# Kernel optimization log

Measured on AMD Instinct MI355X. Metric: run time of the kernel, lower is better.

## Reference

```python
import jax, jax.numpy as jnp
import numpy as np
import math

B, S, D, H, L, V = 16, 512, 1024, 16, 128, 32000
DH = D // H


def _posenc(s, d):
    pos = np.arange(s, dtype=np.float32)[:, None]
    div = np.exp(np.arange(0, d, 2, dtype=np.float32) * (-math.log(10000.0) / d))
    pe = np.zeros((s, d), dtype=np.float32)
    pe[:, 0::2] = np.sin(pos * div)
    pe[:, 1::2] = np.cos(pos * div)
    return jnp.asarray(pe)


def _ln(x, g, b):
    m = jnp.mean(x, axis=-1, keepdims=True)
    v = jnp.mean((x - m) ** 2, axis=-1, keepdims=True)
    return (x - m) / jnp.sqrt(v + 1e-5) * g + b


def setup_inputs():
    key = jax.random.key(0)
    ks = jax.random.split(key, 16)
    w = lambda k, *sh: 0.02 * jax.random.normal(k, sh, dtype=jnp.float32)
    return {
        'x': jax.random.randint(ks[0], (B, S), 0, V),
        'embed': w(ks[1], V, D),
        'Wq': w(ks[2], D, D), 'bq': jnp.zeros((D,), jnp.float32),
        'Wk': w(ks[3], D, D), 'bk': jnp.zeros((D,), jnp.float32),
        'Wv': w(ks[4], D, D), 'bv': jnp.zeros((D,), jnp.float32),
        'Wo': w(ks[5], D, D), 'bo': jnp.zeros((D,), jnp.float32),
        'g1': jnp.ones((D,), jnp.float32), 'be1': jnp.zeros((D,), jnp.float32),
        'W1': w(ks[6], D, D), 'bf1': jnp.zeros((D,), jnp.float32),
        'W2': w(ks[7], D, D), 'bf2': jnp.zeros((D,), jnp.float32),
        'g2': jnp.ones((D,), jnp.float32), 'be2': jnp.zeros((D,), jnp.float32),
        'g3': jnp.ones((D,), jnp.float32), 'be3': jnp.zeros((D,), jnp.float32),
        'Wmu': w(ks[8], D, L), 'bmu': jnp.zeros((L,), jnp.float32),
        'Wsig': w(ks[9], D, L), 'bsig': jnp.zeros((L,), jnp.float32),
        'eps': jax.random.normal(ks[10], (B, S, L), dtype=jnp.float32),
    }


def reference(x, embed, Wq, bq, Wk, bk, Wv, bv, Wo, bo, g1, be1, W1, bf1, W2, bf2,
              g2, be2, g3, be3, Wmu, bmu, Wsig, bsig, eps):
    h = embed[x] * jnp.asarray(D ** 0.5, jnp.float32)          # [B,S,D]
    h = h + _posenc(S, D)                                       # dropout = identity (eval)
    h = _ln(h, g1, be1)
    # attention (faithful to source: raw reshape head-split, scale = dh/2)
    Q = (h @ Wq + bq).reshape(B, H, S, DH)
    K = (h @ Wk + bk).reshape(B, H, S, DH)
    Vv = (h @ Wv + bv).reshape(B, H, S, DH)
    scores = jnp.einsum('bhqd,bhkd->bhqk', Q, K) / (DH / 2.0)
    attn = jax.nn.softmax(scores, axis=-1)
    ctx = jnp.einsum('bhqk,bhkd->bhqd', attn, Vv).reshape(B, S, D)
    ctx = ctx @ Wo + bo
    h = h + ctx
    h = _ln(h, g2, be2)
    f = jax.nn.leaky_relu(h @ W1 + bf1, 0.01) @ W2 + bf2
    h = f + f                                                    # source: x = ffn(x); x = x + drop2(x)
    h = _ln(h, g3, be3)
    mu = h @ Wmu + bmu
    sigma = jnp.exp(h @ Wsig + bsig)
    z = mu + sigma * eps
    return z
```

## Files before the change

### kernel.cpp

```cpp
#include <hip/hip_runtime.h>
#include <cstdint>


typedef __bf16 bf16;
typedef __bf16 bf16x8 __attribute__((ext_vector_type(8)));
typedef __bf16 bf16x4 __attribute__((ext_vector_type(4)));
typedef float f32x4 __attribute__((ext_vector_type(4)));

#define MFMA16(a, b, c) __builtin_amdgcn_mfma_f32_16x16x32_bf16((a), (b), (c), 0, 0, 0)

#if __has_builtin(__builtin_amdgcn_exp2f)
#define EXP2F(x) __builtin_amdgcn_exp2f(x)
#else
#define EXP2F(x) exp2f(x)
#endif

__device__ __forceinline__ void async16(const bf16* g, bf16* l) {
  __builtin_amdgcn_global_load_lds(
      (const __attribute__((address_space(1))) unsigned int*)g,
      (__attribute__((address_space(3))) unsigned int*)l, 16, 0, 0);
}

struct TP6 {
  const float* src[6];
  bf16* dst[6];
};
__global__ __launch_bounds__(256) void transpose6_kernel(TP6 p) {
  const float* __restrict__ W = p.src[blockIdx.z];
  bf16* __restrict__ Wt = p.dst[blockIdx.z];
  __shared__ float tile[64][65];
  const int tk = blockIdx.x * 64, tn = blockIdx.y * 64;
  const int a = threadIdx.x >> 6, b = threadIdx.x & 63;
#pragma unroll
  for (int i = 0; i < 16; ++i) {
    int k = a + i * 4;
    tile[k][b] = W[(size_t)(tk + k) * 1024 + tn + b];
  }
  __syncthreads();
#pragma unroll
  for (int i = 0; i < 16; ++i) {
    int n = a + i * 4;
    Wt[(size_t)(tn + n) * 1024 + tk + b] = (bf16)tile[b][n];
  }
}

__global__ __launch_bounds__(256) void transpose_kernel(const float* __restrict__ W,
                                                        bf16* __restrict__ Wt,
                                                        int K, int N) {
  __shared__ float tile[64][65];
  const int tk = blockIdx.x * 64, tn = blockIdx.y * 64;
  const int a = threadIdx.x >> 6, b = threadIdx.x & 63;
#pragma unroll
  for (int i = 0; i < 16; ++i) {
    int k = a + i * 4;
    tile[k][b] = W[(size_t)(tk + k) * N + tn + b];
  }
  __syncthreads();
#pragma unroll
  for (int i = 0; i < 16; ++i) {
    int n = a + i * 4;
    Wt[(size_t)(tn + n) * K + tk + b] = (bf16)tile[b][n];
  }
}

__global__ __launch_bounds__(256) void embed_ln_kernel(const int* __restrict__ x,
                                                       const float* __restrict__ emb,
                                                       const float* __restrict__ g,
                                                       const float* __restrict__ be,
                                                       bf16* __restrict__ obf,
                                                       float* __restrict__ of) {
  const int row = blockIdx.x;
  const int s = row & 511;
  const int t = x[row];
  const int tid = threadIdx.x;
  const int c = tid * 4;
  const float4 e = *(const float4*)(emb + (size_t)t * 1024 + c);
  const float ev[4] = {e.x, e.y, e.z, e.w};
  float o[4];
#pragma unroll
  for (int j = 0; j < 4; ++j) {
    int cc = c + j;
    float freq = __expf((float)(cc & ~1) * (-9.210340371976184f / 1024.0f));
    float ang = (float)s * freq;
    float pe = (cc & 1) ? cosf(ang) : sinf(ang);
    o[j] = ev[j] * 32.0f + pe;
  }
  float sm = o[0] + o[1] + o[2] + o[3];
  float q = o[0] * o[0] + o[1] * o[1] + o[2] * o[2] + o[3] * o[3];
#pragma unroll
  for (int off = 32; off > 0; off >>= 1) {
    sm += __shfl_down(sm, off);
    q += __shfl_down(q, off);
  }
  __shared__ float rs[4], rq[4];
  const int w = tid >> 6, lane = tid & 63;
  if (lane == 0) { rs[w] = sm; rq[w] = q; }
  __syncthreads();
  const float S = rs[0] + rs[1] + rs[2] + rs[3];
  const float Qs = rq[0] + rq[1] + rq[2] + rq[3];
  const float mean = S * (1.0f / 1024.0f);
  const float var = Qs * (1.0f / 1024.0f) - mean * mean;
  const float rstd = rsqrtf(var + 1e-5f);
  const float4 gv = ((const float4*)g)[tid];
  const float4 bv = ((const float4*)be)[tid];
  const float gvv[4] = {gv.x, gv.y, gv.z, gv.w};
  const float bvv[4] = {bv.x, bv.y, bv.z, bv.w};
  float y[4];
#pragma unroll
  for (int j = 0; j < 4; ++j) y[j] = (o[j] - mean) * rstd * gvv[j] + bvv[j];
  bf16x4 ob = {(bf16)y[0], (bf16)y[1], (bf16)y[2], (bf16)y[3]};
  ((bf16x4*)(obf + (size_t)row * 1024))[tid] = ob;
  float4 o4;  o4.x = y[0]; o4.y = y[1]; o4.z = y[2]; o4.w = y[3];
  ((float4*)(of + (size_t)row * 1024))[tid] = o4;
}

__global__ __launch_bounds__(256) void ln_kernel(const float* __restrict__ in,
                                                 const float* __restrict__ g,
                                                 const float* __restrict__ be,
                                                 bf16* __restrict__ obf,
                                                 float* __restrict__ of) {
  const int row = blockIdx.x;
  const int tid = threadIdx.x;
  const float4 v = ((const float4*)(in + (size_t)row * 1024))[tid];
  float s = v.x + v.y + v.z + v.w;
  float q = v.x * v.x + v.y * v.y + v.z * v.z + v.w * v.w;
#pragma unroll
  for (int off = 32; off > 0; off >>= 1) {
    s += __shfl_down(s, off);
    q += __shfl_down(q, off);
  }
  __shared__ float rs[4], rq[4];
  const int w = tid >> 6, lane = tid & 63;
  if (lane == 0) { rs[w] = s; rq[w] = q; }
  __syncthreads();
  const float S = rs[0] + rs[1] + rs[2] + rs[3];
  const float Qs = rq[0] + rq[1] + rq[2] + rq[3];
  const float mean = S * (1.0f / 1024.0f);
  const float var = Qs * (1.0f / 1024.0f) - mean * mean;
  const float rstd = rsqrtf(var + 1e-5f);
  const float4 gv = ((const float4*)g)[tid];
  const float4 bv = ((const float4*)be)[tid];
  const float y0 = (v.x - mean) * rstd * gv.x + bv.x;
  const float y1 = (v.y - mean) * rstd * gv.y + bv.y;
  const float y2 = (v.z - mean) * rstd * gv.z + bv.z;
  const float y3 = (v.w - mean) * rstd * gv.w + bv.w;
  bf16x4 ob = {(bf16)y0, (bf16)y1, (bf16)y2, (bf16)y3};
  ((bf16x4*)(obf + (size_t)row * 1024))[tid] = ob;
  if (of) {
    float4 o4;  o4.x = y0; o4.y = y1; o4.z = y2; o4.w = y3;
    ((float4*)(of + (size_t)row * 1024))[tid] = o4;
  }
}

template <int MODE>
__global__ __launch_bounds__(256) void gemm_kernel(const bf16* __restrict__ A,
                                                   const bf16* __restrict__ Bt,
                                                   const float* __restrict__ bias,
                                                   void* __restrict__ outv,
                                                   const float* __restrict__ resid,
                                                   int M, int N, int K) {
  __shared__ __attribute__((aligned(16))) bf16 Asm[128 * 32];
  __shared__ __attribute__((aligned(16))) bf16 Bsm[128 * 32];
  const int tid = threadIdx.x;
  const int wv = tid >> 6, lane = tid & 63;
  const int quad = lane >> 4, l15 = lane & 15;
  const int m0 = blockIdx.x * 128, n0 = blockIdx.y * 128;
  const int wm = wv & 1, wn = wv >> 1;

  f32x4 acc[4][4];
#pragma unroll
  for (int i = 0; i < 4; ++i)
#pragma unroll
    for (int j = 0; j < 4; ++j) acc[i][j] = {0.f, 0.f, 0.f, 0.f};

  const int r0 = tid >> 2, c0 = ((tid & 3) ^ ((r0 >> 1) & 3)) * 8;
  const int r1 = (tid + 256) >> 2, c1 = ((tid & 3) ^ ((r1 >> 1) & 3)) * 8;
  const bf16* Ag0 = A + (size_t)(m0 + r0) * K + c0;
  const bf16* Ag1 = A + (size_t)(m0 + r1) * K + c1;
  const bf16* Bg0 = Bt + (size_t)(n0 + r0) * K + c0;
  const bf16* Bg1 = Bt + (size_t)(n0 + r1) * K + c1;
  bf16* lA0 = &Asm[tid * 8];
  bf16* lA1 = &Asm[(tid + 256) * 8];
  bf16* lB0 = &Bsm[tid * 8];
  bf16* lB1 = &Bsm[(tid + 256) * 8];

  for (int k0 = 0; k0 < K; k0 += 32) {
    async16(Ag0 + k0, lA0);
    async16(Ag1 + k0, lA1);
    async16(Bg0 + k0, lB0);
    async16(Bg1 + k0, lB1);
    __syncthreads();
    bf16x8 af[4], bfr[4];
#pragma unroll
    for (int mi = 0; mi < 4; ++mi) {
      const int row = wm * 64 + mi * 16 + l15;
      af[mi] = *(const bf16x8*)(&Asm[(row * 4 + (quad ^ ((row >> 1) & 3))) * 8]);
    }
#pragma unroll
    for (int ni = 0; ni < 4; ++ni) {
      const int row = wn * 64 + ni * 16 + l15;
      bfr[ni] = *(const bf16x8*)(&Bsm[(row * 4 + (quad ^ ((row >> 1) & 3))) * 8]);
    }
#pragma unroll
    for (int mi = 0; mi < 4; ++mi)
#pragma unroll
      for (int ni = 0; ni < 4; ++ni)
        acc[mi][ni] = MFMA16(af[mi], bfr[ni], acc[mi][ni]);
    __syncthreads();
  }

  float* outf = (float*)outv;
  bf16* outb = (bf16*)outv;
#pragma unroll
  for (int ni = 0; ni < 4; ++ni) {
    const int col = n0 + wn * 64 + ni * 16 + l15;
    float bv;
    if constexpr (MODE == 5)
      bv = (col < 128) ? bias[col] : resid[col - 128];
    else
      bv = bias[col];
#pragma unroll
    for (int mi = 0; mi < 4; ++mi) {
#pragma unroll
      for (int r = 0; r < 4; ++r) {
        const int row = m0 + wm * 64 + mi * 16 + quad * 4 + r;
        const size_t idx = (size_t)row * N + col;
        float v = acc[mi][ni][r] + bv;
        if constexpr (MODE == 0) outb[idx] = (bf16)v;
        else if constexpr (MODE == 1) outf[idx] = v + resid[idx];
        else if constexpr (MODE == 2) outb[idx] = (bf16)(v > 0.f ? v : 0.01f * v);
        else if constexpr (MODE == 3) outf[idx] = 2.0f * v;
        else outf[idx] = v;
      }
    }
  }
}

__global__ __launch_bounds__(256) void vtrans_kernel(const bf16* __restrict__ Vb,
                                                     bf16* __restrict__ VtG) {
  __shared__ float t[64][65];
  const int bh = blockIdx.x, kt = blockIdx.y;
  const int tid = threadIdx.x;
  const bf16* src = Vb + (size_t)bh * 32768 + (size_t)kt * 4096;
#pragma unroll
  for (int i = 0; i < 2; ++i) {
    int s = i * 256 + tid;
    int r = s >> 3, c = (s & 7) * 8;
    bf16x8 v = *(const bf16x8*)(src + (size_t)s * 8);
#pragma unroll
    for (int j = 0; j < 8; ++j) t[r][c + j] = (float)v[j];
  }
  __syncthreads();
  bf16* dst = VtG + (size_t)bh * 32768 + kt * 64;
#pragma unroll
  for (int i = 0; i < 2; ++i) {
    int s = i * 256 + tid;
    int d = s >> 3, kc = (s & 7) * 8;
    bf16 tmp[8];
#pragma unroll
    for (int j = 0; j < 8; ++j) tmp[j] = (bf16)t[kc + j][d];
    *(uint4*)(dst + (size_t)d * 512 + kc) = *(const uint4*)tmp;
  }
}

__global__ __launch_bounds__(256) void attn_kernel(const bf16* __restrict__ Qg,
                                                   const bf16* __restrict__ Kg,
                                                   const bf16* __restrict__ Vt,
                                                   bf16* __restrict__ ctx) {
  __shared__ __attribute__((aligned(16))) bf16 Ksm[128 * 64];
  __shared__ __attribute__((aligned(16))) bf16 Vsm[64 * 128];
  __shared__ __attribute__((aligned(16))) bf16 Psm[4][16 * 128];
  const int tid = threadIdx.x;
  const int w = tid >> 6, lane = tid & 63;
  const int quad = lane >> 4, l15 = lane & 15;
  const int bh = blockIdx.x;
  const size_t base = (size_t)bh * 32768;
  const bf16* Vth = Vt + base;
  const int qbase = blockIdx.y * 128 + w * 32;
  const f32x4 fz = {0.f, 0.f, 0.f, 0.f};

  bf16x8 a[2][2];
#pragma unroll
  for (int qt = 0; qt < 2; ++qt)
#pragma unroll
    for (int hf = 0; hf < 2; ++hf) {
      bf16x8 tq = *(const bf16x8*)(Qg + base +
                   (size_t)(qbase + qt * 16 + l15) * 64 + hf * 32 + quad * 8);
#pragma unroll
      for (int e = 0; e < 8; ++e) tq[e] = (bf16)((float)tq[e] * 0.045111758f);
      a[qt][hf] = tq;
    }

  f32x4 o[2][4];
  float l_i[2][4];
#pragma unroll
  for (int qt = 0; qt < 2; ++qt)
#pragma unroll
    for (int i = 0; i < 4; ++i) { o[qt][i] = fz; l_i[qt][i] = 0.f; }

  for (int kv0 = 0; kv0 < 512; kv0 += 128) {
#pragma unroll
    for (int i = 0; i < 4; ++i) {
      int s = i * 256 + tid;
      int r = s >> 3, c = (s & 7) ^ (r & 7);
      async16(Kg + base + (size_t)(kv0 + r) * 64 + c * 8, &Ksm[s * 8]);
    }
#pragma unroll
    for (int i = 0; i < 4; ++i) {
      int s = i * 256 + tid;
      int d = s >> 4, cs = s & 15;
      int c = (cs & 8) | ((cs & 7) ^ (d & 7));
      async16(Vth + (size_t)d * 512 + kv0 + c * 8, &Vsm[s * 8]);
    }
    __syncthreads();

    f32x4 sc[2][8];
#pragma unroll
    for (int j = 0; j < 8; ++j) {
      const int n = j * 16 + l15;
      const bf16x8 k0 = *(const bf16x8*)(&Ksm[(n * 8 + (quad ^ (n & 7))) * 8]);
      const bf16x8 k1 = *(const bf16x8*)(&Ksm[(n * 8 + ((4 + quad) ^ (n & 7))) * 8]);
      sc[0][j] = MFMA16(a[0][0], k0, fz);
      sc[0][j] = MFMA16(a[0][1], k1, sc[0][j]);
      sc[1][j] = MFMA16(a[1][0], k0, fz);
      sc[1][j] = MFMA16(a[1][1], k1, sc[1][j]);
    }

    bf16* ps = &Psm[w][0];
#pragma unroll
    for (int qt = 0; qt < 2; ++qt) {
#pragma unroll
      for (int r = 0; r < 4; ++r) {
        const int prow = quad * 4 + r;
        float sum = 0.f;
#pragma unroll
        for (int j = 0; j < 8; ++j) {
          const float p = EXP2F(sc[qt][j][r]);
          sum += p;
          const int col = j * 16 + l15;
          const int cc = col >> 3;
          const int ccs = (cc & 8) | ((cc & 7) ^ (prow & 7));
          ps[prow * 128 + ccs * 8 + (col & 7)] = (bf16)p;
        }
        l_i[qt][r] += sum;
      }
#pragma unroll
      for (int c32 = 0; c32 < 4; ++c32) {
        const int pc = c32 * 4 + quad;
        const int pcs = (pc & 8) | ((pc & 7) ^ (l15 & 7));
        const bf16x8 pf = *(const bf16x8*)(ps + l15 * 128 + pcs * 8);
#pragma unroll
        for (int ni = 0; ni < 4; ++ni) {
          const int d = ni * 16 + l15;
          const int vcs = (pc & 8) | ((pc & 7) ^ (d & 7));
          const bf16x8 vf = *(const bf16x8*)(&Vsm[(d * 16 + vcs) * 8]);
          o[qt][ni] = MFMA16(pf, vf, o[qt][ni]);
        }
      }
    }
    __syncthreads();
  }

#pragma unroll
  for (int qt = 0; qt < 2; ++qt) {
#pragma unroll
    for (int r = 0; r < 4; ++r) {
      float l = l_i[qt][r];
      l += __shfl_xor(l, 1);
      l += __shfl_xor(l, 2);
      l += __shfl_xor(l, 4);
      l += __shfl_xor(l, 8);
      const float inv = 1.0f / l;
#pragma unroll
      for (int ni = 0; ni < 4; ++ni)
        ctx[base + (size_t)(qbase + qt * 16 + quad * 4 + r) * 64 + ni * 16 + l15]
            = (bf16)(o[qt][ni][r] * inv);
    }
  }
}

__global__ __launch_bounds__(256) void final_kernel(const float* __restrict__ musg,
                                                    const float* __restrict__ eps,
                                                    float* __restrict__ z) {
  const int i = blockIdx.x * 256 + threadIdx.x;
  const int row = i >> 5;
  const int c = (i & 31) * 4;
  const float4 m = *(const float4*)(musg + (size_t)row * 256 + c);
  const float4 s = *(const float4*)(musg + (size_t)row * 256 + 128 + c);
  const float4 e = *(const float4*)(eps + (size_t)row * 128 + c);
  float4 r;
  r.x = m.x + __expf(s.x) * e.x;
  r.y = m.y + __expf(s.y) * e.y;
  r.z = m.z + __expf(s.z) * e.z;
  r.w = m.w + __expf(s.w) * e.w;
  *(float4*)(z + (size_t)row * 128 + c) = r;
}

extern "C" void kernel_launch(void* const* d_in, const int* in_sizes, int n_in,
                              void* d_out, int out_size, void* d_ws, size_t ws_size,
                              hipStream_t stream) {
  (void)in_sizes; (void)n_in; (void)out_size; (void)ws_size;
  const int* x = (const int*)d_in[0];
  const float* emb = (const float*)d_in[1];
  const float* Wq = (const float*)d_in[2];
  const float* bq = (const float*)d_in[3];
  const float* Wk = (const float*)d_in[4];
  const float* bkb = (const float*)d_in[5];
  const float* Wv = (const float*)d_in[6];
  const float* bv = (const float*)d_in[7];
  const float* Wo = (const float*)d_in[8];
  const float* bo = (const float*)d_in[9];
  const float* g1 = (const float*)d_in[10];
  const float* be1 = (const float*)d_in[11];
  const float* W1 = (const float*)d_in[12];
  const float* bf1 = (const float*)d_in[13];
  const float* W2 = (const float*)d_in[14];
  const float* bf2 = (const float*)d_in[15];
  const float* g2 = (const float*)d_in[16];
  const float* be2 = (const float*)d_in[17];
  const float* g3 = (const float*)d_in[18];
  const float* be3 = (const float*)d_in[19];
  const float* Wmu = (const float*)d_in[20];
  const float* bmu = (const float*)d_in[21];
  const float* Wsig = (const float*)d_in[22];
  const float* bsig = (const float*)d_in[23];
  const float* eps = (const float*)d_in[24];
  float* z = (float*)d_out;

  const int M = 8192, D = 1024;
  char* ws = (char*)d_ws;
  size_t off = 0;
  auto alloc = [&](size_t b) {
    char* p = ws + off;
    off += (b + 255) & ~(size_t)255;
    return p;
  };
  bf16* wqT = (bf16*)alloc((size_t)1024 * 1024 * 2);
  bf16* wkT = (bf16*)alloc((size_t)1024 * 1024 * 2);
  bf16* wvT = (bf16*)alloc((size_t)1024 * 1024 * 2);
  bf16* woT = (bf16*)alloc((size_t)1024 * 1024 * 2);
  bf16* w1T = (bf16*)alloc((size_t)1024 * 1024 * 2);
  bf16* w2T = (bf16*)alloc((size_t)1024 * 1024 * 2);
  bf16* wmsT = (bf16*)alloc((size_t)256 * 1024 * 2);
  float* hA = (float*)alloc((size_t)M * D * 4);
  bf16* hb = (bf16*)alloc((size_t)M * D * 2);
  bf16* Qb = (bf16*)alloc((size_t)M * D * 2);
  bf16* Kb = (bf16*)alloc((size_t)M * D * 2);
  bf16* Vb = (bf16*)alloc((size_t)M * D * 2);
  bf16* Cb = (bf16*)alloc((size_t)M * D * 2);
  bf16* VtG = hb;
  float* musg = (float*)Cb;

  dim3 b256(256);
  TP6 tp;
  tp.src[0] = Wq; tp.dst[0] = wqT;
  tp.src[1] = Wk; tp.dst[1] = wkT;
  tp.src[2] = Wv; tp.dst[2] = wvT;
  tp.src[3] = Wo; tp.dst[3] = woT;
  tp.src[4] = W1; tp.dst[4] = w1T;
  tp.src[5] = W2; tp.dst[5] = w2T;
  transpose6_kernel<<<dim3(16, 16, 6), b256, 0, stream>>>(tp);
  transpose_kernel<<<dim3(16, 2), b256, 0, stream>>>(Wmu, wmsT, 1024, 128);
  transpose_kernel<<<dim3(16, 2), b256, 0, stream>>>(Wsig, wmsT + (size_t)128 * 1024, 1024, 128);

  embed_ln_kernel<<<8192, b256, 0, stream>>>(x, emb, g1, be1, hb, hA);

  gemm_kernel<0><<<dim3(64, 8), b256, 0, stream>>>(hb, wqT, bq, Qb, nullptr, M, D, D);
  gemm_kernel<0><<<dim3(64, 8), b256, 0, stream>>>(hb, wkT, bkb, Kb, nullptr, M, D, D);
  gemm_kernel<0><<<dim3(64, 8), b256, 0, stream>>>(hb, wvT, bv, Vb, nullptr, M, D, D);

  vtrans_kernel<<<dim3(256, 8), b256, 0, stream>>>(Vb, VtG);
  attn_kernel<<<dim3(256, 4), b256, 0, stream>>>(Qb, Kb, VtG, Cb);

  gemm_kernel<1><<<dim3(64, 8), b256, 0, stream>>>(Cb, woT, bo, hA, hA, M, D, D);
  ln_kernel<<<8192, b256, 0, stream>>>(hA, g2, be2, hb, nullptr);
  gemm_kernel<2><<<dim3(64, 8), b256, 0, stream>>>(hb, w1T, bf1, Qb, nullptr, M, D, D);
  gemm_kernel<3><<<dim3(64, 8), b256, 0, stream>>>(Qb, w2T, bf2, hA, nullptr, M, D, D);
  ln_kernel<<<8192, b256, 0, stream>>>(hA, g3, be3, hb, nullptr);
  gemm_kernel<5><<<dim3(64, 2), b256, 0, stream>>>(hb, wmsT, bmu, musg, bsig, M, 256, D);
  final_kernel<<<1024, b256, 0, stream>>>(musg, eps, z);
}
```

Before: 506.9 us.

## Fuse QKV GEMM, double-buffer GEMM loads, keep residual stream in bf16

Merges the three Q/K/V projections into one GEMM over a concatenated transposed weight and merges all eight weight transposes into one launch. The GEMM main loop now double-buffers shared-memory tiles so the next k-slice's async loads are issued before the current slice's MFMAs. The fp32 residual/intermediate buffers are replaced with bf16 buffers for the residual add and layernorm inputs, which cuts memory traffic but lowers the precision of the residual path. The in-loop __syncthreads() is kept, so the overlap depends on the compiler not waiting on outstanding async loads at that barrier.

```diff
diff --git a/kernel.cpp b/kernel.cpp
--- a/kernel.cpp
+++ b/kernel.cpp
@@ -21,45 +21,30 @@
       (__attribute__((address_space(3))) unsigned int*)l, 16, 0, 0);
 }
 
-struct TP6 {
-  const float* src[6];
-  bf16* dst[6];
+struct TP8 {
+  const float* src[8];
+  bf16* dst[8];
+  int ncol[8];
 };
-__global__ __launch_bounds__(256) void transpose6_kernel(TP6 p) {
-  const float* __restrict__ W = p.src[blockIdx.z];
-  bf16* __restrict__ Wt = p.dst[blockIdx.z];
+__global__ __launch_bounds__(256) void transpose8_kernel(TP8 p) {
+  const int z = blockIdx.z;
+  const int N = p.ncol[z];
+  const int tk = blockIdx.x * 64, tn = blockIdx.y * 64;
+  if (tn >= N) return;
+  const float* __restrict__ W = p.src[z];
+  bf16* __restrict__ Wt = p.dst[z];
   __shared__ float tile[64][65];
-  const int tk = blockIdx.x * 64, tn = blockIdx.y * 64;
   const int a = threadIdx.x >> 6, b = threadIdx.x & 63;
 #pragma unroll
   for (int i = 0; i < 16; ++i) {
     int k = a + i * 4;
-    tile[k][b] = W[(size_t)(tk + k) * 1024 + tn + b];
+    tile[k][b] = W[(size_t)(tk + k) * N + tn + b];
   }
   __syncthreads();
 #pragma unroll
   for (int i = 0; i < 16; ++i) {
     int n = a + i * 4;
     Wt[(size_t)(tn + n) * 1024 + tk + b] = (bf16)tile[b][n];
-  }
-}
-
-__global__ __launch_bounds__(256) void transpose_kernel(const float* __restrict__ W,
-                                                        bf16* __restrict__ Wt,
-                                                        int K, int N) {
-  __shared__ float tile[64][65];
-  const int tk = blockIdx.x * 64, tn = blockIdx.y * 64;
-  const int a = threadIdx.x >> 6, b = threadIdx.x & 63;
-#pragma unroll
-  for (int i = 0; i < 16; ++i) {
-    int k = a + i * 4;
-    tile[k][b] = W[(size_t)(tk + k) * N + tn + b];
-  }
-  __syncthreads();
-#pragma unroll
-  for (int i = 0; i < 16; ++i) {
-    int n = a + i * 4;
-    Wt[(size_t)(tn + n) * K + tk + b] = (bf16)tile[b][n];
   }
 }
 
@@ -67,8 +52,7 @@
                                                        const float* __restrict__ emb,
                                                        const float* __restrict__ g,
                                                        const float* __restrict__ be,
-                                                       bf16* __restrict__ obf,
-                                                       float* __restrict__ of) {
+                                                       bf16* __restrict__ obf) {
   const int row = blockIdx.x;
   const int s = row & 511;
   const int t = x[row];
@@ -105,25 +89,24 @@
   const float4 bv = ((const float4*)be)[tid];
   const float gvv[4] = {gv.x, gv.y, gv.z, gv.w};
   const float bvv[4] = {bv.x, bv.y, bv.z, bv.w};
-  float y[4];
-#pragma unroll
-  for (int j = 0; j < 4; ++j) y[j] = (o[j] - mean) * rstd * gvv[j] + bvv[j];
-  bf16x4 ob = {(bf16)y[0], (bf16)y[1], (bf16)y[2], (bf16)y[3]};
+  bf16x4 ob;
+#pragma unroll
+  for (int j = 0; j < 4; ++j) ob[j] = (bf16)((o[j] - mean) * rstd * gvv[j] + bvv[j]);
   ((bf16x4*)(obf + (size_t)row * 1024))[tid] = ob;
-  float4 o4;  o4.x = y[0]; o4.y = y[1]; o4.z = y[2]; o4.w = y[3];
-  ((float4*)(of + (size_t)row * 1024))[tid] = o4;
-}
-
-__global__ __launch_bounds__(256) void ln_kernel(const float* __restrict__ in,
+}
+
+__global__ __launch_bounds__(256) void ln_kernel(const bf16* __restrict__ in,
                                                  const float* __restrict__ g,
                                                  const float* __restrict__ be,
-                                                 bf16* __restrict__ obf,
-                                                 float* __restrict__ of) {
+                                                 bf16* __restrict__ obf) {
   const int row = blockIdx.x;
   const int tid = threadIdx.x;
-  const float4 v = ((const float4*)(in + (size_t)row * 1024))[tid];
-  float s = v.x + v.y + v.z + v.w;
-  float q = v.x * v.x + v.y * v.y + v.z * v.z + v.w * v.w;
+  const bf16x4 v4 = ((const bf16x4*)(in + (size_t)row * 1024))[tid];
+  float v[4];
+#pragma unroll
+  for (int j = 0; j < 4; ++j) v[j] = (float)v4[j];
+  float s = v[0] + v[1] + v[2] + v[3];
+  float q = v[0] * v[0] + v[1] * v[1] + v[2] * v[2] + v[3] * v[3];
 #pragma unroll
   for (int off = 32; off > 0; off >>= 1) {
     s += __shfl_down(s, off);
@@ -140,27 +123,24 @@
   const float rstd = rsqrtf(var + 1e-5f);
   const float4 gv = ((const float4*)g)[tid];
   const float4 bv = ((const float4*)be)[tid];
-  const float y0 = (v.x - mean) * rstd * gv.x + bv.x;
-  const float y1 = (v.y - mean) * rstd * gv.y + bv.y;
-  const float y2 = (v.z - mean) * rstd * gv.z + bv.z;
-  const float y3 = (v.w - mean) * rstd * gv.w + bv.w;
-  bf16x4 ob = {(bf16)y0, (bf16)y1, (bf16)y2, (bf16)y3};
+  const float gvv[4] = {gv.x, gv.y, gv.z, gv.w};
+  const float bvv[4] = {bv.x, bv.y, bv.z, bv.w};
+  bf16x4 ob;
+#pragma unroll
+  for (int j = 0; j < 4; ++j) ob[j] = (bf16)((v[j] - mean) * rstd * gvv[j] + bvv[j]);
   ((bf16x4*)(obf + (size_t)row * 1024))[tid] = ob;
-  if (of) {
-    float4 o4;  o4.x = y0; o4.y = y1; o4.z = y2; o4.w = y3;
-    ((float4*)(of + (size_t)row * 1024))[tid] = o4;
-  }
 }
 
 template <int MODE>
-__global__ __launch_bounds__(256) void gemm_kernel(const bf16* __restrict__ A,
-                                                   const bf16* __restrict__ Bt,
-                                                   const float* __restrict__ bias,
-                                                   void* __restrict__ outv,
-                                                   const float* __restrict__ resid,
-                                                   int M, int N, int K) {
-  __shared__ __attribute__((aligned(16))) bf16 Asm[128 * 32];
-  __shared__ __attribute__((aligned(16))) bf16 Bsm[128 * 32];
+__global__ __launch_bounds__(256) void gemm_kernel(
+    const bf16* __restrict__ A, const bf16* __restrict__ Bt,
+    const float* __restrict__ b0f, const float* __restrict__ b1f,
+    const float* __restrict__ b2f,
+    bf16* __restrict__ o0, bf16* __restrict__ o1, bf16* __restrict__ o2,
+    float* __restrict__ of, const bf16* __restrict__ residb,
+    int M, int N, int K) {
+  __shared__ __attribute__((aligned(16))) bf16 Asm[2][128 * 32];
+  __shared__ __attribute__((aligned(16))) bf16 Bsm[2][128 * 32];
   const int tid = threadIdx.x;
   const int wv = tid >> 6, lane = tid & 63;
   const int quad = lane >> 4, l15 = lane & 15;
@@ -179,27 +159,33 @@
   const bf16* Ag1 = A + (size_t)(m0 + r1) * K + c1;
   const bf16* Bg0 = Bt + (size_t)(n0 + r0) * K + c0;
   const bf16* Bg1 = Bt + (size_t)(n0 + r1) * K + c1;
-  bf16* lA0 = &Asm[tid * 8];
-  bf16* lA1 = &Asm[(tid + 256) * 8];
-  bf16* lB0 = &Bsm[tid * 8];
-  bf16* lB1 = &Bsm[(tid + 256) * 8];
-
-  for (int k0 = 0; k0 < K; k0 += 32) {
-    async16(Ag0 + k0, lA0);
-    async16(Ag1 + k0, lA1);
-    async16(Bg0 + k0, lB0);
-    async16(Bg1 + k0, lB1);
-    __syncthreads();
+
+  async16(Ag0, &Asm[0][tid * 8]);
+  async16(Ag1, &Asm[0][(tid + 256) * 8]);
+  async16(Bg0, &Bsm[0][tid * 8]);
+  async16(Bg1, &Bsm[0][(tid + 256) * 8]);
+  __syncthreads();
+
+  const int nk = K >> 5;
+  for (int k = 0; k < nk; ++k) {
+    const int cur = k & 1, nxt = cur ^ 1;
     bf16x8 af[4], bfr[4];
 #pragma unroll
     for (int mi = 0; mi < 4; ++mi) {
       const int row = wm * 64 + mi * 16 + l15;
-      af[mi] = *(const bf16x8*)(&Asm[(row * 4 + (quad ^ ((row >> 1) & 3))) * 8]);
+      af[mi] = *(const bf16x8*)(&Asm[cur][(row * 4 + (quad ^ ((row >> 1) & 3))) * 8]);
     }
 #pragma unroll
     for (int ni = 0; ni < 4; ++ni) {
       const int row = wn * 64 + ni * 16 + l15;
-      bfr[ni] = *(const bf16x8*)(&Bsm[(row * 4 + (quad ^ ((row >> 1) & 3))) * 8]);
+      bfr[ni] = *(const bf16x8*)(&Bsm[cur][(row * 4 + (quad ^ ((row >> 1) & 3))) * 8]);
+    }
+    if (k + 1 < nk) {
+      const int ko = (k + 1) * 32;
+      async16(Ag0 + ko, &Asm[nxt][tid * 8]);
+      async16(Ag1 + ko, &Asm[nxt][(tid + 256) * 8]);
+      async16(Bg0 + ko, &Bsm[nxt][tid * 8]);
+      async16(Bg1 + ko, &Bsm[nxt][(tid + 256) * 8]);
     }
 #pragma unroll
     for (int mi = 0; mi < 4; ++mi)
@@ -209,28 +195,40 @@
     __syncthreads();
   }
 
-  float* outf = (float*)outv;
-  bf16* outb = (bf16*)outv;
+  const int part = (MODE == 6) ? (blockIdx.y >> 3) : 0;
+  bf16* ob = o0;
+  const float* bp = b0f;
+  if constexpr (MODE == 6) {
+    ob = (part == 0) ? o0 : (part == 1 ? o1 : o2);
+    bp = (part == 0) ? b0f : (part == 1 ? b1f : b2f);
+  }
 #pragma unroll
   for (int ni = 0; ni < 4; ++ni) {
     const int col = n0 + wn * 64 + ni * 16 + l15;
+    const int cl = (MODE == 6) ? (col - part * 1024) : col;
     float bv;
     if constexpr (MODE == 5)
-      bv = (col < 128) ? bias[col] : resid[col - 128];
+      bv = (col < 128) ? b0f[col] : b1f[col - 128];
     else
-      bv = bias[col];
+      bv = bp[cl];
 #pragma unroll
     for (int mi = 0; mi < 4; ++mi) {
 #pragma unroll
       for (int r = 0; r < 4; ++r) {
         const int row = m0 + wm * 64 + mi * 16 + quad * 4 + r;
-        const size_t idx = (size_t)row * N + col;
         float v = acc[mi][ni][r] + bv;
-        if constexpr (MODE == 0) outb[idx] = (bf16)v;
-        else if constexpr (MODE == 1) outf[idx] = v + resid[idx];
-        else if constexpr (MODE == 2) outb[idx] = (bf16)(v > 0.f ? v : 0.01f * v);
-        else if constexpr (MODE == 3) outf[idx] = 2.0f * v;
-        else outf[idx] = v;
+        if constexpr (MODE == 1) {
+          const size_t idx = (size_t)row * N + col;
+          o0[idx] = (bf16)(v + (float)residb[idx]);
+        } else if constexpr (MODE == 2) {
+          o0[(size_t)row * N + col] = (bf16)(v > 0.f ? v : 0.01f * v);
+        } else if constexpr (MODE == 3) {
+          o0[(size_t)row * N + col] = (bf16)(2.0f * v);
+        } else if constexpr (MODE == 5) {
+          of[(size_t)row * N + col] = v;
+        } else {
+          ob[(size_t)row * 1024 + cl] = (bf16)v;
+        }
       }
     }
   }
@@ -435,48 +433,57 @@
     off += (b + 255) & ~(size_t)255;
     return p;
   };
-  bf16* wqT = (bf16*)alloc((size_t)1024 * 1024 * 2);
-  bf16* wkT = (bf16*)alloc((size_t)1024 * 1024 * 2);
-  bf16* wvT = (bf16*)alloc((size_t)1024 * 1024 * 2);
+  bf16* wqkvT = (bf16*)alloc((size_t)3072 * 1024 * 2);
   bf16* woT = (bf16*)alloc((size_t)1024 * 1024 * 2);
   bf16* w1T = (bf16*)alloc((size_t)1024 * 1024 * 2);
   bf16* w2T = (bf16*)alloc((size_t)1024 * 1024 * 2);
   bf16* wmsT = (bf16*)alloc((size_t)256 * 1024 * 2);
-  float* hA = (float*)alloc((size_t)M * D * 4);
   bf16* hb = (bf16*)alloc((size_t)M * D * 2);
   bf16* Qb = (bf16*)alloc((size_t)M * D * 2);
   bf16* Kb = (bf16*)alloc((size_t)M * D * 2);
   bf16* Vb = (bf16*)alloc((size_t)M * D * 2);
+  bf16* VtG = (bf16*)alloc((size_t)M * D * 2);
   bf16* Cb = (bf16*)alloc((size_t)M * D * 2);
-  bf16* VtG = hb;
-  float* musg = (float*)Cb;
+  bf16* h2b = (bf16*)alloc((size_t)M * D * 2);
+  bf16* h3b = (bf16*)alloc((size_t)M * D * 2);
+  bf16* hidb = (bf16*)alloc((size_t)M * D * 2);
+  bf16* h4b = (bf16*)alloc((size_t)M * D * 2);
+  bf16* h5b = (bf16*)alloc((size_t)M * D * 2);
+  float* musg = (float*)alloc((size_t)M * 256 * 4);
 
   dim3 b256(256);
-  TP6 tp;
-  tp.src[0] = Wq; tp.dst[0] = wqT;
-  tp.src[1] = Wk; tp.dst[1] = wkT;
-  tp.src[2] = Wv; tp.dst[2] = wvT;
-  tp.src[3] = Wo; tp.dst[3] = woT;
-  tp.src[4] = W1; tp.dst[4] = w1T;
-  tp.src[5] = W2; tp.dst[5] = w2T;
-  transpose6_kernel<<<dim3(16, 16, 6), b256, 0, stream>>>(tp);
-  transpose_kernel<<<dim3(16, 2), b256, 0, stream>>>(Wmu, wmsT, 1024, 128);
-  transpose_kernel<<<dim3(16, 2), b256, 0, stream>>>(Wsig, wmsT + (size_t)128 * 1024, 1024, 128);
-
-  embed_ln_kernel<<<8192, b256, 0, stream>>>(x, emb, g1, be1, hb, hA);
-
-  gemm_kernel<0><<<dim3(64, 8), b256, 0, stream>>>(hb, wqT, bq, Qb, nullptr, M, D, D);
-  gemm_kernel<0><<<dim3(64, 8), b256, 0, stream>>>(hb, wkT, bkb, Kb, nullptr, M, D, D);
-  gemm_kernel<0><<<dim3(64, 8), b256, 0, stream>>>(hb, wvT, bv, Vb, nullptr, M, D, D);
-
+  TP8 tp;
+  tp.src[0] = Wq;   tp.dst[0] = wqkvT;                        tp.ncol[0] = 1024;
+  tp.src[1] = Wk;   tp.dst[1] = wqkvT + (size_t)1024 * 1024;  tp.ncol[1] = 1024;
+  tp.src[2] = Wv;   tp.dst[2] = wqkvT + (size_t)2048 * 1024;  tp.ncol[2] = 1024;
+  tp.src[3] = Wo;   tp.dst[3] = woT;                          tp.ncol[3] = 1024;
+  tp.src[4] = W1;   tp.dst[4] = w1T;                          tp.ncol[4] = 1024;
+  tp.src[5] = W2;   tp.dst[5] = w2T;                          tp.ncol[5] = 1024;
+  tp.src[6] = Wmu;  tp.dst[6] = wmsT;                         tp.ncol[6] = 128;
+  tp.src[7] = Wsig; tp.dst[7] = wmsT + (size_t)128 * 1024;    tp.ncol[7] = 128;
+  transpose8_kernel<<<dim3(16, 16, 8), b256, 0, stream>>>(tp);
+
+  embed_ln_kernel<<<8192, b256, 0, stream>>>(x, emb, g1, be1, hb);
+
+  gemm_kernel<6><<<dim3(64, 24), b256, 0, stream>>>(hb, wqkvT, bq, bkb, bv,
+                                                    Qb, Kb, Vb, nullptr, nullptr,
+                                                    M, 3072, D);
   vtrans_kernel<<<dim3(256, 8), b256, 0, stream>>>(Vb, VtG);
   attn_kernel<<<dim3(256, 4), b256, 0, stream>>>(Qb, Kb, VtG, Cb);
 
-  gemm_kernel<1><<<dim3(64, 8), b256, 0, stream>>>(Cb, woT, bo, hA, hA, M, D, D);
-  ln_kernel<<<8192, b256, 0, stream>>>(hA, g2, be2, hb, nullptr);
-  gemm_kernel<2><<<dim3(64, 8), b256, 0, stream>>>(hb, w1T, bf1, Qb, nullptr, M, D, D);
-  gemm_kernel<3><<<dim3(64, 8), b256, 0, stream>>>(Qb, w2T, bf2, hA, nullptr, M, D, D);
-  ln_kernel<<<8192, b256, 0, stream>>>(hA, g3, be3, hb, nullptr);
-  gemm_kernel<5><<<dim3(64, 2), b256, 0, stream>>>(hb, wmsT, bmu, musg, bsig, M, 256, D);
+  gemm_kernel<1><<<dim3(64, 8), b256, 0, stream>>>(Cb, woT, bo, nullptr, nullptr,
+                                                   h2b, nullptr, nullptr, nullptr, hb,
+                                                   M, D, D);
+  ln_kernel<<<8192, b256, 0, stream>>>(h2b, g2, be2, h3b);
+  gemm_kernel<2><<<dim3(64, 8), b256, 0, stream>>>(h3b, w1T, bf1, nullptr, nullptr,
+                                                   hidb, nullptr, nullptr, nullptr, nullptr,
+                                                   M, D, D);
+  gemm_kernel<3><<<dim3(64, 8), b256, 0, stream>>>(hidb, w2T, bf2, nullptr, nullptr,
+                                                   h4b, nullptr, nullptr, nullptr, nullptr,
+                                                   M, D, D);
+  ln_kernel<<<8192, b256, 0, stream>>>(h4b, g3, be3, h5b);
+  gemm_kernel<5><<<dim3(64, 2), b256, 0, stream>>>(h5b, wmsT, bmu, bsig, nullptr,
+                                                   nullptr, nullptr, nullptr, musg, nullptr,
+                                                   M, 256, D);
   final_kernel<<<1024, b256, 0, stream>>>(musg, eps, z);
 }
```

After: 445.9 us. 12.0% less time.
